# Kernel tuning notes

Hardware: AMD Instinct MI355X
Metric: run time of the kernel (lower is better)

## Reference

```python
import jax, jax.numpy as jnp
import numpy as np

C = 128
B = 64
EPS = 1e-6


def _ln2d(x, w, b):
    # LayerNorm over channel dim (NAFNet-style LayerNorm2d), eps=1e-6
    mu = x.mean(axis=1, keepdims=True)
    var = ((x - mu) ** 2).mean(axis=1, keepdims=True)
    return (x - mu) / jnp.sqrt(var + EPS) * w[None, :, None, None] + b[None, :, None, None]


def _conv4(x, w, b):
    # Conv2d kernel 4, stride 4, no padding; NCHW / OIHW
    y = jax.lax.conv_general_dilated(x, w, (4, 4), 'VALID',
                                     dimension_numbers=('NCHW', 'OIHW', 'NCHW'))
    return y + b[None, :, None, None]


def _pixel_shuffle4(x):
    # (B, c*16, H, W) -> (B, c, 4H, 4W), torch PixelShuffle semantics
    b, c16, h, w = x.shape
    c = c16 // 16
    x = x.reshape(b, c, 4, 4, h, w)
    x = x.transpose(0, 1, 4, 2, 5, 3)
    return x.reshape(b, c, h * 4, w * 4)


def setup_inputs() -> dict:
    key = jax.random.key(0)
    ks = jax.random.split(key, 16)
    s = 0.02
    return {
        'x_l': jax.random.normal(ks[0], (B, C, 32, 32), jnp.float32),
        'x_r': jax.random.normal(ks[1], (B, C, 32, 32), jnp.float32),
        'ln_w_l': jnp.ones((C,), jnp.float32), 'ln_b_l': jnp.zeros((C,), jnp.float32),
        'ln_w_r': jnp.ones((C,), jnp.float32), 'ln_b_r': jnp.zeros((C,), jnp.float32),
        'Wl1': jax.random.normal(ks[2], (C, C, 4, 4), jnp.float32) * s,
        'bl1': jnp.zeros((C,), jnp.float32),
        'Wr1': jax.random.normal(ks[3], (C, C, 4, 4), jnp.float32) * s,
        'br1': jnp.zeros((C,), jnp.float32),
        'Wl2': jax.random.normal(ks[4], (C, C, 4, 4), jnp.float32) * s,
        'bl2': jnp.zeros((C,), jnp.float32),
        'Wr2': jax.random.normal(ks[5], (C, C, 4, 4), jnp.float32) * s,
        'br2': jnp.zeros((C,), jnp.float32),
        'pos': jax.random.normal(ks[6], (1, C, 8, 8), jnp.float32),
        'beta': jax.random.normal(ks[7], (1, C, 1, 1), jnp.float32) * s,
        'gamma': jax.random.normal(ks[8], (1, C, 1, 1), jnp.float32) * s,
        'Wl3': jax.random.normal(ks[9], (16 * C, C), jnp.float32) * s,
        'bl3': jnp.zeros((16 * C,), jnp.float32),
        'Wr3': jax.random.normal(ks[10], (16 * C, C), jnp.float32) * s,
        'br3': jnp.zeros((16 * C,), jnp.float32),
    }


def reference(x_l, x_r, ln_w_l, ln_b_l, ln_w_r, ln_b_r, Wl1, bl1, Wr1, br1,
              Wl2, bl2, Wr2, br2, pos, beta, gamma, Wl3, bl3, Wr3, br3):
    c = x_l.shape[1]
    scale = c ** (-0.5)
    B1 = x_l.shape[0]
    B2 = x_r.shape[0]

    Ql = _conv4(_ln2d(x_l, ln_w_l, ln_b_l), Wl1, bl1) + pos  # (B1,c,8,8)
    Qr = _conv4(_ln2d(x_r, ln_w_r, ln_b_r), Wr1, br1) + pos  # (B2,c,8,8)
    h1, w1 = Ql.shape[-2], Ql.shape[-1]
    h2, w2 = Qr.shape[-2], Qr.shape[-1]
    m1, m2 = h1 * w1, h2 * w2

    Qlm = Ql.transpose(0, 2, 3, 1).reshape(B1, m1, c)          # b (h w) c
    Qrm = Qr.transpose(1, 0, 2, 3).reshape(c, B2 * m2)         # c (b h w)
    Vl = (_conv4(x_l, Wl2, bl2) + pos).transpose(0, 2, 3, 1).reshape(B1 * m1, c)
    Vr = (_conv4(x_r, Wr2, br2) + pos).transpose(0, 2, 3, 1).reshape(B2 * m2, c)

    attn = jnp.matmul(Qlm, Qrm) * scale                        # (B1, m1, B2*m2)

    F_r2l = jnp.matmul(jax.nn.softmax(attn * (B2 ** (-0.5)), axis=-1), Vr)
    F_r2l = F_r2l.reshape(B1, h1, w1, c)

    attn2 = attn.reshape(B1, m1, B2, m2).transpose(2, 3, 0, 1).reshape(B2, m2, B1 * m1)
    F_l2r = jnp.matmul(jax.nn.softmax(attn2 * (B1 ** (-0.5)), axis=-1), Vl)
    F_l2r = F_l2r.reshape(B2, h2, w2, c)

    F_r2l = _pixel_shuffle4((jnp.matmul(F_r2l, Wl3.T) + bl3).transpose(0, 3, 1, 2)) * beta
    F_l2r = _pixel_shuffle4((jnp.matmul(F_l2r, Wr3.T) + br3).transpose(0, 3, 1, 2)) * gamma
    return (x_l + F_r2l, x_r + F_l2r)
```

## Files before the change

kernel.cpp:

```cpp
#include <hip/hip_runtime.h>
#include <stdint.h>

using bf16x8 = __attribute__((ext_vector_type(8))) short;
using f32x4  = __attribute__((ext_vector_type(4))) float;

__device__ __forceinline__ unsigned short f2bf(float f) {
  union { float f; uint32_t u; } v; v.f = f;
  uint32_t r = v.u + 0x7FFFu + ((v.u >> 16) & 1u);
  return (unsigned short)(r >> 16);
}
__device__ __forceinline__ uint32_t pk2(float a, float b) {
  return (uint32_t)f2bf(a) | ((uint32_t)f2bf(b) << 16);
}
__device__ __forceinline__ float bf2f(unsigned short s) {
  union { uint32_t u; float f; } v; v.u = ((uint32_t)s) << 16;
  return v.f;
}
__device__ __forceinline__ f32x4 mfma16(bf16x8 a, bf16x8 b, f32x4 c) {
  return __builtin_amdgcn_mfma_f32_16x16x32_bf16(a, b, c, 0, 0, 0);
}

__global__ __launch_bounds__(256) void k_lnstats(
    const float* __restrict__ xl, const float* __restrict__ xr,
    float* __restrict__ muW, float* __restrict__ rsW)
{
  const int bx = blockIdx.x;
  const int side = bx >> 7, rem = bx & 127;
  const int b = rem >> 1, half = rem & 1;
  const float* x = (side ? xr : xl) + (size_t)b * 131072 + half * 512;
  const int t = threadIdx.x;
  const int px = t * 2;
  float s0=0, s1=0, q0=0, q1=0;
#pragma unroll 4
  for (int c = 0; c < 128; ++c) {
    const float2 v = *(const float2*)(x + c*1024 + px);
    s0 += v.x; q0 += v.x*v.x;
    s1 += v.y; q1 += v.y*v.y;
  }
  const int o = (side*64 + b)*1024 + half*512 + px;
  float2 mu, rs;
  mu.x = s0*(1.0f/128.0f); mu.y = s1*(1.0f/128.0f);
  rs.x = rsqrtf(fmaxf(q0*(1.0f/128.0f) - mu.x*mu.x, 0.0f) + 1e-6f);
  rs.y = rsqrtf(fmaxf(q1*(1.0f/128.0f) - mu.y*mu.y, 0.0f) + 1e-6f);
  *(float2*)(muW + o) = mu;
  *(float2*)(rsW + o) = rs;
}

__global__ __launch_bounds__(256) void k_wprep(
    const float* __restrict__ lnwl, const float* __restrict__ lnbl,
    const float* __restrict__ lnwr, const float* __restrict__ lnbr,
    const float* __restrict__ Wl1, const float* __restrict__ bl1,
    const float* __restrict__ Wr1, const float* __restrict__ br1,
    const float* __restrict__ Wl2, const float* __restrict__ Wr2,
    unsigned short* __restrict__ Wq, unsigned short* __restrict__ Wv,
    float* __restrict__ bqW)
{
  const int bx = blockIdx.x;
  const int side = bx >> 7, co = bx & 127;
  const float* W1  = side ? Wr1 : Wl1;
  const float* W2  = side ? Wr2 : Wl2;
  const float* b1  = side ? br1 : bl1;
  const float* lnw = side ? lnwr : lnwl;
  const float* lnb = side ? lnbr : lnbl;
  const int t = threadIdx.x;
  const int ci = t >> 1;
  const float lw = lnw[ci], lb = lnb[ci];

  const size_t dsto = (size_t)(side*32 + (t>>3))*8192 + (size_t)co*64 + (t&7)*8;

  const float* src1 = W1 + (size_t)co*2048 + t*8;
  const float4 a0 = *(const float4*)(src1);
  const float4 a1 = *(const float4*)(src1 + 4);
  float part = (a0.x+a0.y+a0.z+a0.w + a1.x+a1.y+a1.z+a1.w) * lb;
  uint4 pkq;
  pkq.x = pk2(a0.x*lw, a0.y*lw); pkq.y = pk2(a0.z*lw, a0.w*lw);
  pkq.z = pk2(a1.x*lw, a1.y*lw); pkq.w = pk2(a1.z*lw, a1.w*lw);
  *(uint4*)(Wq + dsto) = pkq;

  const float* src2 = W2 + (size_t)co*2048 + t*8;
  const float4 c0 = *(const float4*)(src2);
  const float4 c1 = *(const float4*)(src2 + 4);
  uint4 pkv;
  pkv.x = pk2(c0.x, c0.y); pkv.y = pk2(c0.z, c0.w);
  pkv.z = pk2(c1.x, c1.y); pkv.w = pk2(c1.z, c1.w);
  *(uint4*)(Wv + dsto) = pkv;

  __shared__ float red[4];
  float v = part;
  v += __shfl_down(v, 32, 64); v += __shfl_down(v, 16, 64);
  v += __shfl_down(v, 8, 64);  v += __shfl_down(v, 4, 64);
  v += __shfl_down(v, 2, 64);  v += __shfl_down(v, 1, 64);
  if ((t & 63) == 0) red[t >> 6] = v;
  __syncthreads();
  if (t == 0) bqW[side*128 + co] = b1[co] + red[0] + red[1] + red[2] + red[3];
}

__global__ __launch_bounds__(256) void k_w3prep(
    const float* __restrict__ Wl3, const float* __restrict__ Wr3,
    unsigned short* __restrict__ W3bf)
{
  const int b = blockIdx.x;
  const float* src = (b < 256 ? Wl3 : Wr3) + (size_t)(b & 255) * 1024;
  const int t = threadIdx.x;
  const float4 v = *(const float4*)(src + t*4);
  *(uint2*)(W3bf + (size_t)b*1024 + t*4) = make_uint2(pk2(v.x, v.y), pk2(v.z, v.w));
}

__global__ __launch_bounds__(256) void k_conv(
    const float* __restrict__ xl, const float* __restrict__ xr,
    const unsigned short* __restrict__ Wq, const unsigned short* __restrict__ Wv,
    const float* __restrict__ muW, const float* __restrict__ rsW,
    unsigned short* __restrict__ Cpart)
{
  const int bid = blockIdx.x;
  const int ks = bid & 3;
  const int img = (bid >> 2) & 63;
  const int ctype = bid >> 8;
  const int side = ctype & 1;
  const bool isQ = ctype < 2;
  const float* x = (side ? xr : xl) + (size_t)img * 131072;
  const unsigned short* Bsrc = (isQ ? Wq : Wv) + (size_t)side * 262144;

  const int t = threadIdx.x;
  const int w = t >> 6, l = t & 63, lo = l & 15, g = l >> 4;

  __shared__ __align__(16) unsigned char lds[24576];
  unsigned char* A = lds;
  unsigned char* B = lds + 8192;

  const int cl   = t >> 6;
  const int px0  = (t & 63) * 16;
  const int y    = px0 >> 5;
  const int wr   = y & 3;
  const int pbase = (y >> 2)*8 + ((px0 & 31) >> 2);

  float4 mu4[4], rs4[4];
  if (isQ) {
    const int o = (side*64 + img)*1024 + px0;
#pragma unroll
    for (int i = 0; i < 4; ++i) {
      mu4[i] = *(const float4*)(muW + o + 4*i);
      rs4[i] = *(const float4*)(rsW + o + 4*i);
    }
  }

  const int cout = t >> 1, part = t & 1;
  const int keyB = ((cout ^ (cout >> 3)) & 7) << 4;

  f32x4 acc[4][2];
#pragma unroll
  for (int a = 0; a < 4; ++a) { acc[a][0] = (f32x4)0.0f; acc[a][1] = (f32x4)0.0f; }

  for (int it = 0; it < 8; ++it) {
    const int kb = ks*8 + it;
    __syncthreads();
    {
      const float* xs = x + (size_t)(kb*4 + cl)*1024 + px0;
#pragma unroll
      for (int i = 0; i < 4; ++i) {
        float4 v = *(const float4*)(xs + 4*i);
        if (isQ) {
          v.x = (v.x - mu4[i].x)*rs4[i].x; v.y = (v.y - mu4[i].y)*rs4[i].y;
          v.z = (v.z - mu4[i].z)*rs4[i].z; v.w = (v.w - mu4[i].w)*rs4[i].w;
        }
        const int p = pbase + i;
        int dst = p*128 + cl*32 + wr*8;
        dst ^= ((p ^ (p >> 3)) & 7) << 4;
        *(uint2*)(A + dst) = make_uint2(pk2(v.x, v.y), pk2(v.z, v.w));
      }
    }
    {
      const unsigned short* bs = Bsrc + (size_t)kb*8192 + t*32;
#pragma unroll
      for (int i = 0; i < 4; ++i) {
        const bf16x8 v = *(const bf16x8*)(bs + i*8);
        *(bf16x8*)(B + cout*128 + ((part*64 + i*16) ^ keyB)) = v;
      }
    }
    __syncthreads();
    bf16x8 af[4][2], bfr[2][2];
#pragma unroll
    for (int mf = 0; mf < 4; ++mf) {
      const int row = mf*16 + lo;
      const int key = ((row ^ (row >> 3)) & 7) << 4;
#pragma unroll
      for (int kc = 0; kc < 2; ++kc)
        af[mf][kc] = *(const bf16x8*)(A + row*128 + ((kc*64 + g*16) ^ key));
    }
#pragma unroll
    for (int nf = 0; nf < 2; ++nf) {
      const int row = w*32 + nf*16 + lo;
      const int key = ((row ^ (row >> 3)) & 7) << 4;
#pragma unroll
      for (int kc = 0; kc < 2; ++kc)
        bfr[nf][kc] = *(const bf16x8*)(B + row*128 + ((kc*64 + g*16) ^ key));
    }
    __builtin_amdgcn_s_setprio(1);
#pragma unroll
    for (int kc = 0; kc < 2; ++kc)
#pragma unroll
      for (int nf = 0; nf < 2; ++nf)
#pragma unroll
        for (int mf = 0; mf < 4; ++mf)
          acc[mf][nf] = mfma16(af[mf][kc], bfr[nf][kc], acc[mf][nf]);
    __builtin_amdgcn_s_setprio(0);
  }

  unsigned short* Cp = Cpart + (size_t)bid * 8192;
#pragma unroll
  for (int mf = 0; mf < 4; ++mf)
#pragma unroll
    for (int nf = 0; nf < 2; ++nf) {
      const int c = w*32 + nf*16 + lo;
      const int p0 = mf*16 + g*4;
      *(uint2*)(Cp + c*64 + p0) =
          make_uint2(pk2(acc[mf][nf][0], acc[mf][nf][1]),
                     pk2(acc[mf][nf][2], acc[mf][nf][3]));
    }
}

__global__ __launch_bounds__(256) void k_convred(
    const unsigned short* __restrict__ Cpart,
    const float* __restrict__ bqW,
    const float* __restrict__ bl2, const float* __restrict__ br2,
    const float* __restrict__ pos,
    unsigned short* __restrict__ Qbf, unsigned short* __restrict__ Vtbf)
{
  const int bid2 = blockIdx.x;
  const int ctype = bid2 >> 6, img = bid2 & 63;
  const int side = ctype & 1;
  const bool isQ = ctype < 2;
  const int t = threadIdx.x;

  __shared__ float S[64][130];

  const int c = t >> 1, p0 = (t & 1) * 32;
  {
    float acc[32];
#pragma unroll
    for (int j = 0; j < 32; ++j) acc[j] = 0.f;
#pragma unroll
    for (int s = 0; s < 4; ++s) {
      const unsigned short* Cp = Cpart + ((size_t)(bid2*4 + s))*8192 + c*64 + p0;
#pragma unroll
      for (int j8 = 0; j8 < 4; ++j8) {
        const bf16x8 v = *(const bf16x8*)(Cp + j8*8);
#pragma unroll
        for (int e = 0; e < 8; ++e)
          acc[j8*8 + e] += bf2f((unsigned short)v[e]);
      }
    }
#pragma unroll
    for (int j = 0; j < 32; ++j) S[p0 + j][c] = acc[j];
  }
  __syncthreads();

  if (isQ) {
    const float* bq = bqW + side*128;
    const int p = t >> 2, c0 = (t & 3) * 32;
    const int rot = (t & 3) * 4;
    uint32_t pk[16];
#pragma unroll
    for (int j2 = 0; j2 < 16; ++j2) {
      const int jj = (j2 + rot) & 15;
      const int ca = c0 + jj*2;
      const float2 sv = *(const float2*)(&S[p][ca]);
      const float va = (sv.x + bq[ca]     + pos[ca*64 + p])     * 0.105112052f;
      const float vb = (sv.y + bq[ca + 1] + pos[(ca+1)*64 + p]) * 0.105112052f;
      pk[jj] = pk2(va, vb);
    }
    unsigned short* Qo = Qbf + (size_t)side*524288 + ((size_t)(img*64 + p))*128 + c0;
    *(uint4*)(Qo)      = make_uint4(pk[0],  pk[1],  pk[2],  pk[3]);
    *(uint4*)(Qo + 8)  = make_uint4(pk[4],  pk[5],  pk[6],  pk[7]);
    *(uint4*)(Qo + 16) = make_uint4(pk[8],  pk[9],  pk[10], pk[11]);
    *(uint4*)(Qo + 24) = make_uint4(pk[12], pk[13], pk[14], pk[15]);
  } else {
    const float* b2 = side ? br2 : bl2;
    const float bb = b2[c];
    uint32_t pk[16];
#pragma unroll
    for (int j2 = 0; j2 < 16; ++j2) {
      const int pa = p0 + j2*2;
      const float va = S[pa][c]     + bb + pos[c*64 + pa];
      const float vb = S[pa + 1][c] + bb + pos[c*64 + pa + 1];
      pk[j2] = pk2(va, vb);
    }
    unsigned short* Vo = Vtbf + (size_t)side*524288 + (size_t)c*4096 + img*64 + p0;
    *(uint4*)(Vo)      = make_uint4(pk[0],  pk[1],  pk[2],  pk[3]);
    *(uint4*)(Vo + 8)  = make_uint4(pk[4],  pk[5],  pk[6],  pk[7]);
    *(uint4*)(Vo + 16) = make_uint4(pk[8],  pk[9],  pk[10], pk[11]);
    *(uint4*)(Vo + 24) = make_uint4(pk[12], pk[13], pk[14], pk[15]);
  }
}

__global__ __launch_bounds__(256, 2) void k_attn(
    const unsigned short* __restrict__ Qbf,
    const unsigned short* __restrict__ Vtbf,
    float* __restrict__ Opart,
    float* __restrict__ Lpart)
{
  const int qb = blockIdx.x, ks = blockIdx.y, dir = blockIdx.z;
  const unsigned short* Qp = Qbf  + (size_t)dir*524288;
  const unsigned short* Kp = Qbf  + (size_t)(1-dir)*524288;
  const unsigned short* Vp = Vtbf + (size_t)(1-dir)*524288;

  const int t = threadIdx.x;
  const int w = t >> 6, l = t & 63, lo = l & 15, g = l >> 4;

  __shared__ __align__(16) unsigned char lds[73728];
  unsigned char* ldsP = lds + 65536;
  __shared__ float lred[4][64];

  bf16x8 aq[4][4];
#pragma unroll
  for (int mf = 0; mf < 4; ++mf)
#pragma unroll
    for (int kc = 0; kc < 4; ++kc)
      aq[mf][kc] = *(const bf16x8*)(Qp + (size_t)(qb*64 + mf*16 + lo)*128 + kc*32 + g*8);

  f32x4 o[4][2];
#pragma unroll
  for (int a = 0; a < 4; ++a) { o[a][0] = (f32x4)0.0f; o[a][1] = (f32x4)0.0f; }
  float ls[4][4] = {{0,0,0,0},{0,0,0,0},{0,0,0,0},{0,0,0,0}};

  const int kt0 = ks * 16;

  const int ksrcBase = t ^ ((t >> 4) & 7);
  const int vc    = t >> 3;
  const int vi16  = (t & 7) * 16;
  const int vsoff = (vi16 ^ (((t >> 3) & 7) << 4)) >> 1;

  {
    const uint4* src = (const uint4*)(Kp + (size_t)kt0*8192);
#pragma unroll
    for (int j = 0; j < 4; ++j)
      *(uint4*)(lds + (t + 256*j)*16) = src[ksrcBase + 256*j];
#pragma unroll
    for (int j = 0; j < 4; ++j) {
      const int c = vc + 32*j;
      *(uint4*)(lds + 32768 + c*128 + vi16) =
          *(const uint4*)(Vp + (size_t)c*4096 + kt0*64 + vsoff);
    }
  }
  __syncthreads();

  for (int it = 0; it < 16; ++it) {
    const int cur = it & 1;
    unsigned char* curK = lds + cur*16384;
    unsigned char* curV = lds + 32768 + cur*16384;

    uint4 kr0, kr1, kr2, kr3, vr0, vr1, vr2, vr3;
    if (it < 15) {
      const int kt = kt0 + it + 1;
      const uint4* src = (const uint4*)(Kp + (size_t)kt*8192);
      kr0 = src[ksrcBase];
      kr1 = src[ksrcBase + 256];
      kr2 = src[ksrcBase + 512];
      kr3 = src[ksrcBase + 768];
      const unsigned short* vsrc = Vp + (size_t)kt*64 + vsoff;
      vr0 = *(const uint4*)(vsrc + (size_t)(vc     )*4096);
      vr1 = *(const uint4*)(vsrc + (size_t)(vc + 32)*4096);
      vr2 = *(const uint4*)(vsrc + (size_t)(vc + 64)*4096);
      vr3 = *(const uint4*)(vsrc + (size_t)(vc + 96)*4096);
    }

    f32x4 s[4];
    s[0] = (f32x4)0.0f; s[1] = (f32x4)0.0f; s[2] = (f32x4)0.0f; s[3] = (f32x4)0.0f;
    const int krow = w*16 + lo;
    const int keyk = (krow & 7) << 4;
    __builtin_amdgcn_s_setprio(1);
#pragma unroll
    for (int kc = 0; kc < 4; ++kc) {
      const bf16x8 bk = *(const bf16x8*)(curK + krow*256 + ((kc*64 + g*16) ^ keyk));
#pragma unroll
      for (int mf = 0; mf < 4; ++mf)
        s[mf] = mfma16(aq[mf][kc], bk, s[mf]);
    }
    __builtin_amdgcn_s_setprio(0);

#pragma unroll
    for (int mf = 0; mf < 4; ++mf)
#pragma unroll
      for (int rr = 0; rr < 4; ++rr) {
        const float e = __expf(s[mf][rr]);
        ls[mf][rr] += e;
        const int q = mf*16 + g*4 + rr;
        const int inrow = (w*32 + lo*2) ^ ((q & 7) << 4);
        *(unsigned short*)(ldsP + q*128 + inrow) = f2bf(e);
      }
    __syncthreads();

    __builtin_amdgcn_s_setprio(1);
#pragma unroll
    for (int kd = 0; kd < 2; ++kd) {
      bf16x8 pa[4];
#pragma unroll
      for (int mf = 0; mf < 4; ++mf) {
        const int q = mf*16 + lo;
        pa[mf] = *(const bf16x8*)(ldsP + q*128 + ((kd*64 + g*16) ^ ((q & 7) << 4)));
      }
#pragma unroll
      for (int nf = 0; nf < 2; ++nf) {
        const int c = w*32 + nf*16 + lo;
        const bf16x8 bv = *(const bf16x8*)(curV + c*128 + ((kd*64 + g*16) ^ ((c & 7) << 4)));
#pragma unroll
        for (int mf = 0; mf < 4; ++mf)
          o[mf][nf] = mfma16(pa[mf], bv, o[mf][nf]);
      }
    }
    __builtin_amdgcn_s_setprio(0);

    if (it < 15) {
      unsigned char* nK = lds + (cur ^ 1)*16384;
      unsigned char* nV = lds + 32768 + (cur ^ 1)*16384;
      *(uint4*)(nK + (t      )*16) = kr0;
      *(uint4*)(nK + (t + 256)*16) = kr1;
      *(uint4*)(nK + (t + 512)*16) = kr2;
      *(uint4*)(nK + (t + 768)*16) = kr3;
      *(uint4*)(nV + (vc     )*128 + vi16) = vr0;
      *(uint4*)(nV + (vc + 32)*128 + vi16) = vr1;
      *(uint4*)(nV + (vc + 64)*128 + vi16) = vr2;
      *(uint4*)(nV + (vc + 96)*128 + vi16) = vr3;
    }
    __syncthreads();
  }

#pragma unroll
  for (int mf = 0; mf < 4; ++mf)
#pragma unroll
    for (int rr = 0; rr < 4; ++rr) {
      float v = ls[mf][rr];
      v += __shfl_xor(v, 1, 64);
      v += __shfl_xor(v, 2, 64);
      v += __shfl_xor(v, 4, 64);
      v += __shfl_xor(v, 8, 64);
      ls[mf][rr] = v;
    }
  if (lo == 0) {
#pragma unroll
    for (int mf = 0; mf < 4; ++mf)
#pragma unroll
      for (int rr = 0; rr < 4; ++rr)
        lred[w][mf*16 + g*4 + rr] = ls[mf][rr];
  }
  __syncthreads();

  float* Ob = Opart + (((size_t)dir*64 + qb)*4 + ks)*64*128;
#pragma unroll
  for (int mf = 0; mf < 4; ++mf)
#pragma unroll
    for (int nf = 0; nf < 2; ++nf) {
      const int c = w*32 + nf*16 + lo;
#pragma unroll
      for (int rr = 0; rr < 4; ++rr) {
        const int q = mf*16 + g*4 + rr;
        Ob[q*128 + c] = o[mf][nf][rr];
      }
    }
  if (t < 64)
    Lpart[(((size_t)dir*64 + qb)*4 + ks)*64 + t] =
        lred[0][t] + lred[1][t] + lred[2][t] + lred[3][t];
}

__global__ __launch_bounds__(256) void k_reduce(
    const float* __restrict__ Opart, const float* __restrict__ Lpart,
    unsigned short* __restrict__ Fbf)
{
  const int bid = blockIdx.x;
  const int dir = bid >> 7, rb = bid & 127;
  const int t = threadIdx.x;
  const int qr = t >> 3;
  const int cs = (t & 7) * 16;
  const int r  = rb*32 + qr;
  const int qb = r >> 6, q = r & 63;
  const size_t pb = ((size_t)dir*64 + qb)*4;
  float acc[16];
#pragma unroll
  for (int i = 0; i < 16; ++i) acc[i] = 0.f;
  float lsum = 0.f;
#pragma unroll
  for (int s = 0; s < 4; ++s) {
    const float* Ob = Opart + ((pb + s)*64 + q)*128 + cs;
#pragma unroll
    for (int i = 0; i < 16; i += 4) {
      const float4 v = *(const float4*)(Ob + i);
      acc[i] += v.x; acc[i+1] += v.y; acc[i+2] += v.z; acc[i+3] += v.w;
    }
    lsum += Lpart[(pb + s)*64 + q];
  }
  const float inv = 1.0f / lsum;
  uint32_t pkw[8];
#pragma unroll
  for (int i = 0; i < 8; ++i) pkw[i] = pk2(acc[2*i]*inv, acc[2*i+1]*inv);
  unsigned short* Fo = Fbf + (size_t)dir*524288 + (size_t)r*128 + cs;
  *(uint4*)(Fo)     = make_uint4(pkw[0], pkw[1], pkw[2], pkw[3]);
  *(uint4*)(Fo + 8) = make_uint4(pkw[4], pkw[5], pkw[6], pkw[7]);
}

__global__ __launch_bounds__(256) void k_proj(
    const unsigned short* __restrict__ Fbf,
    const unsigned short* __restrict__ W3bf,
    const float* __restrict__ bl3, const float* __restrict__ br3,
    const float* __restrict__ beta, const float* __restrict__ gamma,
    const float* __restrict__ xl, const float* __restrict__ xr,
    float* __restrict__ out)
{
  const int nb = blockIdx.x, mb = blockIdx.y, side = blockIdx.z;
  const unsigned short* F  = Fbf + (size_t)side*524288 + (size_t)mb*8192;
  const unsigned short* W3 = W3bf + (size_t)side*262144 + (size_t)nb*16384;
  const float* b3  = (side ? br3 : bl3) + nb*128;
  const float* scl = side ? gamma : beta;
  const float* xin = (side ? xr : xl) + (size_t)mb*131072;
  float* op = out + (size_t)side*8388608 + (size_t)mb*131072;

  const int t = threadIdx.x;
  const int w = t >> 6, l = t & 63, lo = l & 15, g = l >> 4;

  __shared__ __align__(16) unsigned char lds[49152];
  unsigned char* Ft = lds;
  unsigned char* B3 = lds + 16384;
  float* Sf = (float*)lds;

  {
    const uint4* src = (const uint4*)F;
#pragma unroll
    for (int j = 0; j < 4; ++j) {
      const int idx = t + 256*j;
      const int dst = idx*16;
      const int row = dst >> 8;
      *(uint4*)(Ft + dst) = src[(dst ^ ((row & 7) << 4)) >> 4];
    }
  }
  {
    const int nl = t >> 1, half = t & 1;
    const unsigned short* wsrc = W3 + (size_t)nl*128 + half*64;
#pragma unroll
    for (int ch = 0; ch < 8; ++ch) {
      const uint4 v = *(const uint4*)(wsrc + ch*8);
      const int inrow = (half*128 + ch*16) ^ ((nl & 7) << 4);
      *(uint4*)(B3 + nl*256 + inrow) = v;
    }
  }
  __syncthreads();

  f32x4 acc[4][2];
#pragma unroll
  for (int a=0;a<4;a++) { acc[a][0] = (f32x4)0.0f; acc[a][1] = (f32x4)0.0f; }

  bf16x8 af[4][4];
#pragma unroll
  for (int mf = 0; mf < 4; ++mf) {
    const int row = mf*16 + lo;
#pragma unroll
    for (int kc = 0; kc < 4; ++kc)
      af[mf][kc] = *(const bf16x8*)(Ft + row*256 + ((kc*64 + g*16) ^ ((row & 7) << 4)));
  }
#pragma unroll
  for (int kc = 0; kc < 4; ++kc)
#pragma unroll
    for (int nf = 0; nf < 2; ++nf) {
      const int n = w*32 + nf*16 + lo;
      const bf16x8 bb = *(const bf16x8*)(B3 + n*256 + ((kc*64 + g*16) ^ ((n & 7) << 4)));
#pragma unroll
      for (int mf = 0; mf < 4; ++mf)
        acc[mf][nf] = mfma16(af[mf][kc], bb, acc[mf][nf]);
    }

  __syncthreads();

  {
    const int r4 = (lo >> 2) & 3, sc = lo & 3;
#pragma unroll
    for (int nf = 0; nf < 2; ++nf) {
      const int cl = w*2 + nf;
      const int n16 = w*32 + nf*16 + lo;
      const float scc = scl[nb*8 + cl];
      const float bb3 = b3[n16];
#pragma unroll
      for (int mf = 0; mf < 4; ++mf)
#pragma unroll
        for (int rr = 0; rr < 4; ++rr) {
          const int pi = mf*16 + g*4 + rr;
          const int h = pi >> 3, wc = pi & 7;
          Sf[cl*1032 + h*128 + r4*32 + wc*4 + sc] = scc*(acc[mf][nf][rr] + bb3);
        }
    }
  }
  __syncthreads();

#pragma unroll
  for (int j = 0; j < 8; ++j) {
    const int pix = t*4;
    const float4 s = *(const float4*)(Sf + j*1032 + pix);
    const size_t gaddr = (size_t)(nb*8 + j)*1024 + pix;
    const float4 xv = *(const float4*)(xin + gaddr);
    float4 r;
    r.x = xv.x + s.x; r.y = xv.y + s.y; r.z = xv.z + s.z; r.w = xv.w + s.w;
    *(float4*)(op + gaddr) = r;
  }
}

extern "C" void kernel_launch(void* const* d_in, const int* in_sizes, int n_in,
                              void* d_out, int out_size, void* d_ws, size_t ws_size,
                              hipStream_t stream) {
  (void)in_sizes; (void)n_in; (void)out_size; (void)ws_size;
  const float* xl   = (const float*)d_in[0];
  const float* xr   = (const float*)d_in[1];
  const float* lnwl = (const float*)d_in[2];
  const float* lnbl = (const float*)d_in[3];
  const float* lnwr = (const float*)d_in[4];
  const float* lnbr = (const float*)d_in[5];
  const float* Wl1  = (const float*)d_in[6];
  const float* bl1  = (const float*)d_in[7];
  const float* Wr1  = (const float*)d_in[8];
  const float* br1  = (const float*)d_in[9];
  const float* Wl2  = (const float*)d_in[10];
  const float* bl2  = (const float*)d_in[11];
  const float* Wr2  = (const float*)d_in[12];
  const float* br2  = (const float*)d_in[13];
  const float* pos  = (const float*)d_in[14];
  const float* beta = (const float*)d_in[15];
  const float* gamma= (const float*)d_in[16];
  const float* Wl3  = (const float*)d_in[17];
  const float* bl3  = (const float*)d_in[18];
  const float* Wr3  = (const float*)d_in[19];
  const float* br3  = (const float*)d_in[20];

  float* muW = (float*)d_ws;
  float* rsW = muW + 131072;
  float* bqW = rsW + 131072;
  unsigned short* Wq   = (unsigned short*)(bqW + 256);
  unsigned short* Wv   = Wq + 524288;
  unsigned short* Qbf  = Wv + 524288;
  unsigned short* Vtbf = Qbf + 1048576;
  unsigned short* Fbf  = Vtbf + 1048576;
  unsigned short* W3bf = Fbf + 1048576;
  unsigned short* Cpart = W3bf + 524288;
  float* Opart = (float*)Cpart;
  float* Lpart = (float*)(Cpart + 8388608);

  k_lnstats<<<256, 256, 0, stream>>>(xl, xr, muW, rsW);
  k_wprep<<<256, 256, 0, stream>>>(lnwl, lnbl, lnwr, lnbr,
      Wl1, bl1, Wr1, br1, Wl2, Wr2, Wq, Wv, bqW);
  k_w3prep<<<512, 256, 0, stream>>>(Wl3, Wr3, W3bf);
  k_conv<<<1024, 256, 0, stream>>>(xl, xr, Wq, Wv, muW, rsW, Cpart);
  k_convred<<<256, 256, 0, stream>>>(Cpart, bqW, bl2, br2, pos, Qbf, Vtbf);
  k_attn<<<dim3(64, 4, 2), 256, 0, stream>>>(Qbf, Vtbf, Opart, Lpart);
  k_reduce<<<256, 256, 0, stream>>>(Opart, Lpart, Fbf);
  k_proj<<<dim3(16, 64, 2), 256, 0, stream>>>(Fbf, W3bf, bl3, br3,
      beta, gamma, xl, xr, (float*)d_out);
}
```

Before: 121.6 us.

## Software-pipeline attention QK and PV stages with single V buffer and XCD-aware grid

Restructures the attention loop so the QK^T/exp stage of tile it overlaps the PV MFMA of tile it-1, with a double-buffered P tile and K prefetched two tiles ahead. One barrier per iteration replaces two, and V uses a single LDS buffer with a new row-contiguous load pattern. The grid becomes 1-D with block ids mapped so that (dir, ks) pairs share an XCD for L2 reuse of K/V. Opart/Lpart traffic uses nontemporal stores and loads. This adds prologue/epilogue complexity and carries a risk of register pressure under launch bounds of 2 blocks per CU.

```diff
diff --git a/kernel.cpp b/kernel.cpp
--- a/kernel.cpp
+++ b/kernel.cpp
@@ -299,7 +299,11 @@
     float* __restrict__ Opart,
     float* __restrict__ Lpart)
 {
-  const int qb = blockIdx.x, ks = blockIdx.y, dir = blockIdx.z;
+  const int bid = blockIdx.x;
+  const int xcd = bid & 7;
+  const int dir = xcd >> 2;
+  const int ks  = xcd & 3;
+  const int qb  = bid >> 3;
   const unsigned short* Qp = Qbf  + (size_t)dir*524288;
   const unsigned short* Kp = Qbf  + (size_t)(1-dir)*524288;
   const unsigned short* Vp = Vtbf + (size_t)(1-dir)*524288;
@@ -307,8 +311,8 @@
   const int t = threadIdx.x;
   const int w = t >> 6, l = t & 63, lo = l & 15, g = l >> 4;
 
-  __shared__ __align__(16) unsigned char lds[73728];
-  unsigned char* ldsP = lds + 65536;
+  __shared__ __align__(16) unsigned char lds[65536];
+  unsigned char* Vb = lds + 32768;
   __shared__ float lred[4][64];
 
   bf16x8 aq[4][4];
@@ -324,60 +328,46 @@
   float ls[4][4] = {{0,0,0,0},{0,0,0,0},{0,0,0,0},{0,0,0,0}};
 
   const int kt0 = ks * 16;
-
   const int ksrcBase = t ^ ((t >> 4) & 7);
-  const int vc    = t >> 3;
-  const int vi16  = (t & 7) * 16;
-  const int vsoff = (vi16 ^ (((t >> 3) & 7) << 4)) >> 1;
+  const int vrow  = w*32 + (l >> 1);
+  const int vhalf = l & 1;
+  const int vkey  = (vrow & 7) << 4;
+  const int krow = w*16 + lo;
+  const int keyk = (krow & 7) << 4;
+
+  uint4 kr0, kr1, kr2, kr3, vr0, vr1, vr2, vr3;
 
   {
     const uint4* src = (const uint4*)(Kp + (size_t)kt0*8192);
 #pragma unroll
     for (int j = 0; j < 4; ++j)
       *(uint4*)(lds + (t + 256*j)*16) = src[ksrcBase + 256*j];
-#pragma unroll
-    for (int j = 0; j < 4; ++j) {
-      const int c = vc + 32*j;
-      *(uint4*)(lds + 32768 + c*128 + vi16) =
-          *(const uint4*)(Vp + (size_t)c*4096 + kt0*64 + vsoff);
-    }
+    const unsigned short* vs = Vp + (size_t)vrow*4096 + kt0*64 + vhalf*32;
+#pragma unroll
+    for (int j = 0; j < 4; ++j)
+      *(uint4*)(Vb + vrow*128 + ((vhalf*64 + j*16) ^ vkey)) = *(const uint4*)(vs + j*8);
+  }
+  {
+    const uint4* src = (const uint4*)(Kp + (size_t)(kt0+1)*8192);
+    kr0 = src[ksrcBase]; kr1 = src[ksrcBase+256]; kr2 = src[ksrcBase+512]; kr3 = src[ksrcBase+768];
+    const unsigned short* vs = Vp + (size_t)vrow*4096 + (kt0+1)*64 + vhalf*32;
+    vr0 = *(const uint4*)(vs); vr1 = *(const uint4*)(vs+8); vr2 = *(const uint4*)(vs+16); vr3 = *(const uint4*)(vs+24);
   }
   __syncthreads();
 
-  for (int it = 0; it < 16; ++it) {
-    const int cur = it & 1;
-    unsigned char* curK = lds + cur*16384;
-    unsigned char* curV = lds + 32768 + cur*16384;
-
-    uint4 kr0, kr1, kr2, kr3, vr0, vr1, vr2, vr3;
-    if (it < 15) {
-      const int kt = kt0 + it + 1;
-      const uint4* src = (const uint4*)(Kp + (size_t)kt*8192);
-      kr0 = src[ksrcBase];
-      kr1 = src[ksrcBase + 256];
-      kr2 = src[ksrcBase + 512];
-      kr3 = src[ksrcBase + 768];
-      const unsigned short* vsrc = Vp + (size_t)kt*64 + vsoff;
-      vr0 = *(const uint4*)(vsrc + (size_t)(vc     )*4096);
-      vr1 = *(const uint4*)(vsrc + (size_t)(vc + 32)*4096);
-      vr2 = *(const uint4*)(vsrc + (size_t)(vc + 64)*4096);
-      vr3 = *(const uint4*)(vsrc + (size_t)(vc + 96)*4096);
-    }
-
+  {
     f32x4 s[4];
     s[0] = (f32x4)0.0f; s[1] = (f32x4)0.0f; s[2] = (f32x4)0.0f; s[3] = (f32x4)0.0f;
-    const int krow = w*16 + lo;
-    const int keyk = (krow & 7) << 4;
     __builtin_amdgcn_s_setprio(1);
 #pragma unroll
     for (int kc = 0; kc < 4; ++kc) {
-      const bf16x8 bk = *(const bf16x8*)(curK + krow*256 + ((kc*64 + g*16) ^ keyk));
+      const bf16x8 bk = *(const bf16x8*)(lds + krow*256 + ((kc*64 + g*16) ^ keyk));
 #pragma unroll
       for (int mf = 0; mf < 4; ++mf)
         s[mf] = mfma16(aq[mf][kc], bk, s[mf]);
     }
     __builtin_amdgcn_s_setprio(0);
-
+    unsigned char* Pb = lds + 49152;
 #pragma unroll
     for (int mf = 0; mf < 4; ++mf)
 #pragma unroll
@@ -386,43 +376,114 @@
         ls[mf][rr] += e;
         const int q = mf*16 + g*4 + rr;
         const int inrow = (w*32 + lo*2) ^ ((q & 7) << 4);
-        *(unsigned short*)(ldsP + q*128 + inrow) = f2bf(e);
-      }
-    __syncthreads();
-
-    __builtin_amdgcn_s_setprio(1);
-#pragma unroll
-    for (int kd = 0; kd < 2; ++kd) {
-      bf16x8 pa[4];
-#pragma unroll
-      for (int mf = 0; mf < 4; ++mf) {
-        const int q = mf*16 + lo;
-        pa[mf] = *(const bf16x8*)(ldsP + q*128 + ((kd*64 + g*16) ^ ((q & 7) << 4)));
-      }
-#pragma unroll
-      for (int nf = 0; nf < 2; ++nf) {
-        const int c = w*32 + nf*16 + lo;
-        const bf16x8 bv = *(const bf16x8*)(curV + c*128 + ((kd*64 + g*16) ^ ((c & 7) << 4)));
-#pragma unroll
-        for (int mf = 0; mf < 4; ++mf)
-          o[mf][nf] = mfma16(pa[mf], bv, o[mf][nf]);
-      }
-    }
-    __builtin_amdgcn_s_setprio(0);
-
+        *(unsigned short*)(Pb + q*128 + inrow) = f2bf(e);
+      }
+  }
+  {
+    unsigned char* nK = lds + 16384;
+    *(uint4*)(nK + (t      )*16) = kr0;
+    *(uint4*)(nK + (t + 256)*16) = kr1;
+    *(uint4*)(nK + (t + 512)*16) = kr2;
+    *(uint4*)(nK + (t + 768)*16) = kr3;
+    const uint4* src = (const uint4*)(Kp + (size_t)(kt0+2)*8192);
+    kr0 = src[ksrcBase]; kr1 = src[ksrcBase+256]; kr2 = src[ksrcBase+512]; kr3 = src[ksrcBase+768];
+  }
+  __syncthreads();
+
+  for (int it = 1; it < 16; ++it) {
     if (it < 15) {
-      unsigned char* nK = lds + (cur ^ 1)*16384;
-      unsigned char* nV = lds + 32768 + (cur ^ 1)*16384;
+      unsigned char* nK = lds + ((it + 1) & 1)*16384;
       *(uint4*)(nK + (t      )*16) = kr0;
       *(uint4*)(nK + (t + 256)*16) = kr1;
       *(uint4*)(nK + (t + 512)*16) = kr2;
       *(uint4*)(nK + (t + 768)*16) = kr3;
-      *(uint4*)(nV + (vc     )*128 + vi16) = vr0;
-      *(uint4*)(nV + (vc + 32)*128 + vi16) = vr1;
-      *(uint4*)(nV + (vc + 64)*128 + vi16) = vr2;
-      *(uint4*)(nV + (vc + 96)*128 + vi16) = vr3;
+    }
+    if (it < 14) {
+      const uint4* src = (const uint4*)(Kp + (size_t)(kt0 + it + 2)*8192);
+      kr0 = src[ksrcBase]; kr1 = src[ksrcBase+256]; kr2 = src[ksrcBase+512]; kr3 = src[ksrcBase+768];
+    }
+
+    {
+      unsigned char* curK = lds + (it & 1)*16384;
+      f32x4 s[4];
+      s[0] = (f32x4)0.0f; s[1] = (f32x4)0.0f; s[2] = (f32x4)0.0f; s[3] = (f32x4)0.0f;
+      __builtin_amdgcn_s_setprio(1);
+#pragma unroll
+      for (int kc = 0; kc < 4; ++kc) {
+        const bf16x8 bk = *(const bf16x8*)(curK + krow*256 + ((kc*64 + g*16) ^ keyk));
+#pragma unroll
+        for (int mf = 0; mf < 4; ++mf)
+          s[mf] = mfma16(aq[mf][kc], bk, s[mf]);
+      }
+      __builtin_amdgcn_s_setprio(0);
+      unsigned char* Pb = lds + 49152 + (it & 1)*8192;
+#pragma unroll
+      for (int mf = 0; mf < 4; ++mf)
+#pragma unroll
+        for (int rr = 0; rr < 4; ++rr) {
+          const float e = __expf(s[mf][rr]);
+          ls[mf][rr] += e;
+          const int q = mf*16 + g*4 + rr;
+          const int inrow = (w*32 + lo*2) ^ ((q & 7) << 4);
+          *(unsigned short*)(Pb + q*128 + inrow) = f2bf(e);
+        }
+    }
+
+    {
+      unsigned char* Pp = lds + 49152 + ((it - 1) & 1)*8192;
+      __builtin_amdgcn_s_setprio(1);
+#pragma unroll
+      for (int kd = 0; kd < 2; ++kd) {
+        bf16x8 pa[4];
+#pragma unroll
+        for (int mf = 0; mf < 4; ++mf) {
+          const int q = mf*16 + lo;
+          pa[mf] = *(const bf16x8*)(Pp + q*128 + ((kd*64 + g*16) ^ ((q & 7) << 4)));
+        }
+#pragma unroll
+        for (int nf = 0; nf < 2; ++nf) {
+          const int c = w*32 + nf*16 + lo;
+          const bf16x8 bv = *(const bf16x8*)(Vb + c*128 + ((kd*64 + g*16) ^ ((c & 7) << 4)));
+#pragma unroll
+          for (int mf = 0; mf < 4; ++mf)
+            o[mf][nf] = mfma16(pa[mf], bv, o[mf][nf]);
+        }
+      }
+      __builtin_amdgcn_s_setprio(0);
+    }
+
+    *(uint4*)(Vb + vrow*128 + ((vhalf*64 +  0) ^ vkey)) = vr0;
+    *(uint4*)(Vb + vrow*128 + ((vhalf*64 + 16) ^ vkey)) = vr1;
+    *(uint4*)(Vb + vrow*128 + ((vhalf*64 + 32) ^ vkey)) = vr2;
+    *(uint4*)(Vb + vrow*128 + ((vhalf*64 + 48) ^ vkey)) = vr3;
+    if (it < 15) {
+      const unsigned short* vs = Vp + (size_t)vrow*4096 + (kt0 + it + 1)*64 + vhalf*32;
+      vr0 = *(const uint4*)(vs); vr1 = *(const uint4*)(vs+8); vr2 = *(const uint4*)(vs+16); vr3 = *(const uint4*)(vs+24);
     }
     __syncthreads();
+  }
+
+  {
+    unsigned char* Pp = lds + 49152 + 8192;
+    __builtin_amdgcn_s_setprio(1);
+#pragma unroll
+    for (int kd = 0; kd < 2; ++kd) {
+      bf16x8 pa[4];
+#pragma unroll
+      for (int mf = 0; mf < 4; ++mf) {
+        const int q = mf*16 + lo;
+        pa[mf] = *(const bf16x8*)(Pp + q*128 + ((kd*64 + g*16) ^ ((q & 7) << 4)));
+      }
+#pragma unroll
+      for (int nf = 0; nf < 2; ++nf) {
+        const int c = w*32 + nf*16 + lo;
+        const bf16x8 bv = *(const bf16x8*)(Vb + c*128 + ((kd*64 + g*16) ^ ((c & 7) << 4)));
+#pragma unroll
+        for (int mf = 0; mf < 4; ++mf)
+          o[mf][nf] = mfma16(pa[mf], bv, o[mf][nf]);
+      }
+    }
+    __builtin_amdgcn_s_setprio(0);
   }
 
 #pragma unroll
@@ -454,12 +515,13 @@
 #pragma unroll
       for (int rr = 0; rr < 4; ++rr) {
         const int q = mf*16 + g*4 + rr;
-        Ob[q*128 + c] = o[mf][nf][rr];
+        __builtin_nontemporal_store(o[mf][nf][rr], &Ob[q*128 + c]);
       }
     }
   if (t < 64)
-    Lpart[(((size_t)dir*64 + qb)*4 + ks)*64 + t] =
-        lred[0][t] + lred[1][t] + lred[2][t] + lred[3][t];
+    __builtin_nontemporal_store(
+        lred[0][t] + lred[1][t] + lred[2][t] + lred[3][t],
+        &Lpart[(((size_t)dir*64 + qb)*4 + ks)*64 + t]);
 }
 
 __global__ __launch_bounds__(256) void k_reduce(
@@ -483,8 +545,8 @@
     const float* Ob = Opart + ((pb + s)*64 + q)*128 + cs;
 #pragma unroll
     for (int i = 0; i < 16; i += 4) {
-      const float4 v = *(const float4*)(Ob + i);
-      acc[i] += v.x; acc[i+1] += v.y; acc[i+2] += v.z; acc[i+3] += v.w;
+      const f32x4 v = __builtin_nontemporal_load((const f32x4*)(Ob + i));
+      acc[i] += v[0]; acc[i+1] += v[1]; acc[i+2] += v[2]; acc[i+3] += v[3];
     }
     lsum += Lpart[(pb + s)*64 + q];
   }
@@ -645,7 +707,7 @@
   k_w3prep<<<512, 256, 0, stream>>>(Wl3, Wr3, W3bf);
   k_conv<<<1024, 256, 0, stream>>>(xl, xr, Wq, Wv, muW, rsW, Cpart);
   k_convred<<<256, 256, 0, stream>>>(Cpart, bqW, bl2, br2, pos, Qbf, Vtbf);
-  k_attn<<<dim3(64, 4, 2), 256, 0, stream>>>(Qbf, Vtbf, Opart, Lpart);
+  k_attn<<<512, 256, 0, stream>>>(Qbf, Vtbf, Opart, Lpart);
   k_reduce<<<256, 256, 0, stream>>>(Opart, Lpart, Fbf);
   k_proj<<<dim3(16, 64, 2), 256, 0, stream>>>(Fbf, W3bf, bl3, br3,
       beta, gamma, xl, xr, (float*)d_out);
```

Result: slower. 125.2 us (+3.0%).

## Fuse Q and V conv blocks to share input loads; remap attention grid for XCD locality

Applied to the files above, without the earlier changes.

Each conv block now computes both the LayerNorm-applied Q projection and the raw V projection from a single load of the input tile. Both bf16 A tiles and both weight tiles are staged in a larger LDS buffer, and the grid is halved. This removes the duplicate global read of x_l/x_r but doubles LDS use and the accumulator registers per block, which may reduce occupancy. Separately, the attention kernel moves to a 1D grid whose low three block-index bits pick direction and key split, so blocks that share K/V data are placed on the same XCD and can reuse its L2 cache.

```diff
diff --git a/kernel.cpp b/kernel.cpp
--- a/kernel.cpp
+++ b/kernel.cpp
@@ -115,18 +115,15 @@
   const int bid = blockIdx.x;
   const int ks = bid & 3;
   const int img = (bid >> 2) & 63;
-  const int ctype = bid >> 8;
-  const int side = ctype & 1;
-  const bool isQ = ctype < 2;
+  const int side = bid >> 8;
   const float* x = (side ? xr : xl) + (size_t)img * 131072;
-  const unsigned short* Bsrc = (isQ ? Wq : Wv) + (size_t)side * 262144;
+  const unsigned short* BQsrc = Wq + (size_t)side * 262144;
+  const unsigned short* BVsrc = Wv + (size_t)side * 262144;
 
   const int t = threadIdx.x;
   const int w = t >> 6, l = t & 63, lo = l & 15, g = l >> 4;
 
-  __shared__ __align__(16) unsigned char lds[24576];
-  unsigned char* A = lds;
-  unsigned char* B = lds + 8192;
+  __shared__ __align__(16) unsigned char lds[49152];
 
   const int cl   = t >> 6;
   const int px0  = (t & 63) * 16;
@@ -135,7 +132,7 @@
   const int pbase = (y >> 2)*8 + ((px0 & 31) >> 2);
 
   float4 mu4[4], rs4[4];
-  if (isQ) {
+  {
     const int o = (side*64 + img)*1024 + px0;
 #pragma unroll
     for (int i = 0; i < 4; ++i) {
@@ -147,9 +144,12 @@
   const int cout = t >> 1, part = t & 1;
   const int keyB = ((cout ^ (cout >> 3)) & 7) << 4;
 
-  f32x4 acc[4][2];
-#pragma unroll
-  for (int a = 0; a < 4; ++a) { acc[a][0] = (f32x4)0.0f; acc[a][1] = (f32x4)0.0f; }
+  f32x4 accq[4][2], accv[4][2];
+#pragma unroll
+  for (int a = 0; a < 4; ++a) {
+    accq[a][0] = (f32x4)0.0f; accq[a][1] = (f32x4)0.0f;
+    accv[a][0] = (f32x4)0.0f; accv[a][1] = (f32x4)0.0f;
+  }
 
   for (int it = 0; it < 8; ++it) {
     const int kb = ks*8 + it;
@@ -158,42 +158,50 @@
       const float* xs = x + (size_t)(kb*4 + cl)*1024 + px0;
 #pragma unroll
       for (int i = 0; i < 4; ++i) {
-        float4 v = *(const float4*)(xs + 4*i);
-        if (isQ) {
-          v.x = (v.x - mu4[i].x)*rs4[i].x; v.y = (v.y - mu4[i].y)*rs4[i].y;
-          v.z = (v.z - mu4[i].z)*rs4[i].z; v.w = (v.w - mu4[i].w)*rs4[i].w;
-        }
+        const float4 v = *(const float4*)(xs + 4*i);
         const int p = pbase + i;
         int dst = p*128 + cl*32 + wr*8;
         dst ^= ((p ^ (p >> 3)) & 7) << 4;
-        *(uint2*)(A + dst) = make_uint2(pk2(v.x, v.y), pk2(v.z, v.w));
+        *(uint2*)(lds + 8192 + dst) = make_uint2(pk2(v.x, v.y), pk2(v.z, v.w));
+        float4 q;
+        q.x = (v.x - mu4[i].x)*rs4[i].x; q.y = (v.y - mu4[i].y)*rs4[i].y;
+        q.z = (v.z - mu4[i].z)*rs4[i].z; q.w = (v.w - mu4[i].w)*rs4[i].w;
+        *(uint2*)(lds + dst) = make_uint2(pk2(q.x, q.y), pk2(q.z, q.w));
       }
     }
     {
-      const unsigned short* bs = Bsrc + (size_t)kb*8192 + t*32;
+      const unsigned short* bq = BQsrc + (size_t)kb*8192 + t*32;
+      const unsigned short* bv = BVsrc + (size_t)kb*8192 + t*32;
 #pragma unroll
       for (int i = 0; i < 4; ++i) {
-        const bf16x8 v = *(const bf16x8*)(bs + i*8);
-        *(bf16x8*)(B + cout*128 + ((part*64 + i*16) ^ keyB)) = v;
+        const int dst = cout*128 + ((part*64 + i*16) ^ keyB);
+        *(bf16x8*)(lds + 16384 + dst) = *(const bf16x8*)(bq + i*8);
+        *(bf16x8*)(lds + 32768 + dst) = *(const bf16x8*)(bv + i*8);
       }
     }
     __syncthreads();
-    bf16x8 af[4][2], bfr[2][2];
+    bf16x8 afq[4][2], afv[4][2], bfq[2][2], bfv[2][2];
 #pragma unroll
     for (int mf = 0; mf < 4; ++mf) {
       const int row = mf*16 + lo;
       const int key = ((row ^ (row >> 3)) & 7) << 4;
 #pragma unroll
-      for (int kc = 0; kc < 2; ++kc)
-        af[mf][kc] = *(const bf16x8*)(A + row*128 + ((kc*64 + g*16) ^ key));
+      for (int kc = 0; kc < 2; ++kc) {
+        const int off = row*128 + ((kc*64 + g*16) ^ key);
+        afq[mf][kc] = *(const bf16x8*)(lds + off);
+        afv[mf][kc] = *(const bf16x8*)(lds + 8192 + off);
+      }
     }
 #pragma unroll
     for (int nf = 0; nf < 2; ++nf) {
       const int row = w*32 + nf*16 + lo;
       const int key = ((row ^ (row >> 3)) & 7) << 4;
 #pragma unroll
-      for (int kc = 0; kc < 2; ++kc)
-        bfr[nf][kc] = *(const bf16x8*)(B + row*128 + ((kc*64 + g*16) ^ key));
+      for (int kc = 0; kc < 2; ++kc) {
+        const int off = row*128 + ((kc*64 + g*16) ^ key);
+        bfq[nf][kc] = *(const bf16x8*)(lds + 16384 + off);
+        bfv[nf][kc] = *(const bf16x8*)(lds + 32768 + off);
+      }
     }
     __builtin_amdgcn_s_setprio(1);
 #pragma unroll
@@ -201,21 +209,27 @@
 #pragma unroll
       for (int nf = 0; nf < 2; ++nf)
 #pragma unroll
-        for (int mf = 0; mf < 4; ++mf)
-          acc[mf][nf] = mfma16(af[mf][kc], bfr[nf][kc], acc[mf][nf]);
+        for (int mf = 0; mf < 4; ++mf) {
+          accq[mf][nf] = mfma16(afq[mf][kc], bfq[nf][kc], accq[mf][nf]);
+          accv[mf][nf] = mfma16(afv[mf][kc], bfv[nf][kc], accv[mf][nf]);
+        }
     __builtin_amdgcn_s_setprio(0);
   }
 
-  unsigned short* Cp = Cpart + (size_t)bid * 8192;
+  unsigned short* CpQ = Cpart + ((size_t)((side*64 + img)*4 + ks)) * 8192;
+  unsigned short* CpV = Cpart + ((size_t)(((2 + side)*64 + img)*4 + ks)) * 8192;
 #pragma unroll
   for (int mf = 0; mf < 4; ++mf)
 #pragma unroll
     for (int nf = 0; nf < 2; ++nf) {
       const int c = w*32 + nf*16 + lo;
       const int p0 = mf*16 + g*4;
-      *(uint2*)(Cp + c*64 + p0) =
-          make_uint2(pk2(acc[mf][nf][0], acc[mf][nf][1]),
-                     pk2(acc[mf][nf][2], acc[mf][nf][3]));
+      *(uint2*)(CpQ + c*64 + p0) =
+          make_uint2(pk2(accq[mf][nf][0], accq[mf][nf][1]),
+                     pk2(accq[mf][nf][2], accq[mf][nf][3]));
+      *(uint2*)(CpV + c*64 + p0) =
+          make_uint2(pk2(accv[mf][nf][0], accv[mf][nf][1]),
+                     pk2(accv[mf][nf][2], accv[mf][nf][3]));
     }
 }
 
@@ -299,7 +313,11 @@
     float* __restrict__ Opart,
     float* __restrict__ Lpart)
 {
-  const int qb = blockIdx.x, ks = blockIdx.y, dir = blockIdx.z;
+  const int bid = blockIdx.x;
+  const int xcd = bid & 7;
+  const int dir = xcd >> 2;
+  const int ks  = xcd & 3;
+  const int qb  = bid >> 3;
   const unsigned short* Qp = Qbf  + (size_t)dir*524288;
   const unsigned short* Kp = Qbf  + (size_t)(1-dir)*524288;
   const unsigned short* Vp = Vtbf + (size_t)(1-dir)*524288;
@@ -643,9 +661,9 @@
   k_wprep<<<256, 256, 0, stream>>>(lnwl, lnbl, lnwr, lnbr,
       Wl1, bl1, Wr1, br1, Wl2, Wr2, Wq, Wv, bqW);
   k_w3prep<<<512, 256, 0, stream>>>(Wl3, Wr3, W3bf);
-  k_conv<<<1024, 256, 0, stream>>>(xl, xr, Wq, Wv, muW, rsW, Cpart);
+  k_conv<<<512, 256, 0, stream>>>(xl, xr, Wq, Wv, muW, rsW, Cpart);
   k_convred<<<256, 256, 0, stream>>>(Cpart, bqW, bl2, br2, pos, Qbf, Vtbf);
-  k_attn<<<dim3(64, 4, 2), 256, 0, stream>>>(Qbf, Vtbf, Opart, Lpart);
+  k_attn<<<512, 256, 0, stream>>>(Qbf, Vtbf, Opart, Lpart);
   k_reduce<<<256, 256, 0, stream>>>(Opart, Lpart, Fbf);
   k_proj<<<dim3(16, 64, 2), 256, 0, stream>>>(Fbf, W3bf, bl3, br3,
       beta, gamma, xl, xr, (float*)d_out);
```

Result: slower. 136.9 us (+12.6%).
